# Kernel optimization log

Hardware: AMD Instinct MI355X
Metric: run time of the kernel (lower is better)

The kernel has to match this reference:

```python
import jax, jax.numpy as jnp
import numpy as np

# Geometry constants fixed by the source's index arithmetic
GRID_P, GRID_Q, NUM_ANCH = 60, 40, 9   # p = (i//9)%60, q = i//(60*9), sr = i%9
N = GRID_P * GRID_Q * NUM_ANCH          # 21600 anchors per image
K = 1000                                # top-K candidates kept before NMS
MAX_BOXES = 18                          # fixed output boxes per image
THRESH = 0.5                            # NMS overlap threshold
BATCH = 64


def setup_inputs() -> dict:
    key = jax.random.key(0)
    k1, k2 = jax.random.split(key)
    x = jax.random.normal(k1, (BATCH, N, 6), dtype=jnp.float32)
    # anchor boxes (x, y, w, h); keep w,h strictly positive and away from 0
    anchor_boxes = jax.random.uniform(k2, (GRID_P, GRID_Q, NUM_ANCH, 4),
                                      dtype=jnp.float32, minval=0.05, maxval=1.0)
    return {"x": x, "anchor_boxes": anchor_boxes}


def _per_sample(ypred, anchors):
    scores, order = jax.lax.top_k(ypred[:, 0], K)          # descending, matches tf.argsort DESC [:1000]
    p = (order // NUM_ANCH) % GRID_P
    q = order // (GRID_P * NUM_ANCH)
    sr = order % NUM_ANCH
    a = anchors[p, q, sr]                                   # [K, 4] (xa, ya, wa, ha)
    regr = ypred[order, 2:6]                                # [K, 4] (dx, dy, dw, dh)
    xc = regr[:, 0] * a[:, 2] + a[:, 0]
    yc = regr[:, 1] * a[:, 3] + a[:, 1]
    w = a[:, 2] * jnp.exp(regr[:, 2])
    h = a[:, 3] * jnp.exp(regr[:, 3])
    cand = jnp.stack([xc, yc, w, h, scores], axis=-1)       # [K, 5] xywh+score

    # xywh -> xyxy for overlap computation (as in non_max_suppression_fast)
    x1 = xc - 0.5 * w; x2 = xc + 0.5 * w
    y1 = yc - 0.5 * h; y2 = yc + 0.5 * h
    area = (x2 - x1) * (y2 - y1)                            # [K]

    # pairwise intersection; overlap[i, j] = inter(i, j) / area(j)  (source divides by
    # the area of the lower-scored candidate, NOT the union -- kept faithfully)
    xx1 = jnp.maximum(x1[:, None], x1[None, :])
    yy1 = jnp.maximum(y1[:, None], y1[None, :])
    xx2 = jnp.minimum(x2[:, None], x2[None, :])
    yy2 = jnp.minimum(y2[:, None], y2[None, :])
    iw = jnp.maximum(0.0, xx2 - xx1)
    ih = jnp.maximum(0.0, yy2 - yy1)
    sup = (iw * ih / area[None, :]) > THRESH                # [K, K] bool

    # greedy NMS over candidates in descending-score order
    jrange = jnp.arange(K)
    def body(i, keep):
        return keep & ~(keep[i] & sup[i] & (jrange > i))
    keep = jax.lax.fori_loop(0, K, body, jnp.ones((K,), dtype=bool))

    # pack first MAX_BOXES kept boxes into fixed-shape output
    ranks = jnp.cumsum(keep) - 1                            # position among kept
    valid = keep & (ranks < MAX_BOXES)
    picked = jnp.zeros((MAX_BOXES, 5), cand.dtype).at[
        jnp.where(valid, ranks, MAX_BOXES)
    ].set(jnp.where(valid[:, None], cand, 0.0), mode='drop')

    # pad with top-scored decoded boxes if fewer than MAX_BOXES survive NMS
    n = jnp.minimum(jnp.sum(keep), MAX_BOXES)
    j = jnp.arange(MAX_BOXES)
    pad = cand[jnp.clip(j - n, 0, K - 1)]
    return jnp.where((j < n)[:, None], picked, pad)         # [MAX_BOXES, 5]


def reference(x, anchor_boxes):
    return jax.vmap(lambda y: _per_sample(y, anchor_boxes))(x)  # [B, 18, 5]
```

## Files before the change

### kernel.cpp

```cpp
#include <hip/hip_runtime.h>

#define NELEM 21600
#define KSEL 1000
#define MAXB 18
#define NT 1024
#define CAP 2048
#define NBIN 6144
#define BSHIFT 12
#define NCHUNK 4
#define QC 8100
#define QK 5400
#define NFULL 21
#define NTAIL (NELEM - NFULL * NT)

typedef unsigned long long ull;

__device__ __forceinline__ unsigned fkey(float f) {
  unsigned u = __float_as_uint(f);
  return (u & 0x80000000u) ? ~u : (u | 0x80000000u);
}
__device__ __forceinline__ float unfkey(unsigned k) {
  unsigned u = (k & 0x80000000u) ? (k ^ 0x80000000u) : ~k;
  return __uint_as_float(u);
}

__global__ __launch_bounds__(NT) void k1_scan(
    const float* __restrict__ x, unsigned* __restrict__ gkeys,
    unsigned* __restrict__ ghist, unsigned* __restrict__ gcnt,
    unsigned* __restrict__ gflag) {
  const int blk = blockIdx.x;
  const int s = blk >> 2, c = blk & 3;
  const int t = threadIdx.x;
  const float4* xq = (const float4*)(x + (size_t)s * NELEM * 6);
  unsigned* gk = gkeys + (size_t)s * NELEM;

  __shared__ unsigned h[2048];
  h[2 * t] = 0u; h[2 * t + 1] = 0u;
  if (c == 0 && t == 0) { gcnt[s] = 0u; gflag[s] = 0u; }
  __syncthreads();

  const int base = c * QC;
  #pragma unroll
  for (int k = 0; k < 8; ++k) {
    int off = t + (k << 10);
    if (k < 7 || off < QC) {
      int g = base + off;
      float4 v = xq[g];
      int r = g % 3;
      if (r == 0) {
        unsigned key = fkey(v.x);
        gk[2 * (g / 3)] = key;
        atomicAdd(&h[key >> 21], 1u);
      } else if (r == 1) {
        unsigned key = fkey(v.z);
        gk[2 * (g / 3) + 1] = key;
        atomicAdd(&h[key >> 21], 1u);
      }
    }
  }
  __syncthreads();
  unsigned* gh = ghist + (size_t)blk * 2048;
  gh[2 * t] = h[2 * t];
  gh[2 * t + 1] = h[2 * t + 1];
}

__device__ void select_bucket(const unsigned* hist, unsigned target,
                              volatile unsigned* chunkSuf,
                              unsigned* outB, unsigned* outCnt, unsigned* outAbove) {
  const int tid = threadIdx.x;
  const int w = tid >> 6, l = tid & 63;
  unsigned h1 = hist[w * 128 + 2 * l + 1];
  unsigned s = hist[w * 128 + 2 * l] + h1;
  #pragma unroll
  for (int d = 1; d < 64; d <<= 1) {
    unsigned t = __shfl_down(s, d);
    if (l + d < 64) s += t;
  }
  if (l == 0) chunkSuf[w] = s;
  __syncthreads();
  if (w == 0) {
    unsigned ct = (l < 16) ? chunkSuf[l] : 0u;
    unsigned cs = ct;
    #pragma unroll
    for (int d = 1; d < 16; d <<= 1) {
      unsigned t = __shfl_down(cs, d);
      if (l + d < 16) cs += t;
    }
    if (l < 16) chunkSuf[l] = cs - ct;
  }
  __syncthreads();
  unsigned base = chunkSuf[w];
  unsigned sufE = s + base;
  unsigned sN = __shfl_down(s, 1);
  unsigned sufN = ((l < 63) ? sN : 0u) + base;
  unsigned geOdd = sufN + h1;
  if (sufE >= target && geOdd < target) { *outB = w * 128u + 2u * l;     *outCnt = sufE;  *outAbove = geOdd; }
  if (geOdd >= target && sufN < target) { *outB = w * 128u + 2u * l + 1; *outCnt = geOdd; *outAbove = sufN;  }
  __syncthreads();
}

__global__ __launch_bounds__(NT) void k2_compact(
    const unsigned* __restrict__ gkeys, const unsigned* __restrict__ ghist,
    ull* __restrict__ gselPk, unsigned* __restrict__ gcnt,
    unsigned* __restrict__ gflag, unsigned* __restrict__ gtb) {
  const int blk = blockIdx.x;
  const int s = blk >> 2, q = blk & 3;
  const int tid = threadIdx.x;

  __shared__ unsigned hist[2048];
  __shared__ unsigned chunkSuf[16];
  __shared__ ull lbuf[CAP];
  __shared__ unsigned lcnt, gbase;
  __shared__ unsigned sB, sCnt, sAbove;

  {
    unsigned h0 = 0, h1 = 0;
    #pragma unroll
    for (int c = 0; c < NCHUNK; ++c) {
      const unsigned* gh = ghist + (size_t)(s * NCHUNK + c) * 2048;
      h0 += gh[2 * tid];
      h1 += gh[2 * tid + 1];
    }
    hist[2 * tid] = h0; hist[2 * tid + 1] = h1;
  }
  if (tid == 0) lcnt = 0u;
  __syncthreads();
  select_bucket(hist, KSEL, chunkSuf, &sB, &sCnt, &sAbove);

  if (sCnt > (unsigned)CAP) {
    if (tid == 0 && q == 0) gflag[s] = 1u;
    return;
  }
  const unsigned TB = sB << 21;
  if (tid == 0 && q == 0) gtb[s] = TB;
  const unsigned* ks = gkeys + (size_t)s * NELEM + q * QK;
  const int lw = tid & 63;
  #pragma unroll
  for (int it = 0; it < 6; ++it) {
    int i = tid + (it << 10);
    bool pred = false;
    unsigned k = 0u;
    if (i < QK) { k = ks[i]; pred = (k >= TB); }
    ull mask = __ballot(pred);
    if (mask) {
      int leader = __builtin_ctzll(mask);
      unsigned tot = (unsigned)__popcll(mask);
      unsigned bp = 0;
      if (lw == leader) bp = atomicAdd(&lcnt, tot);
      bp = __shfl(bp, leader);
      if (pred) {
        unsigned p = bp + (unsigned)__popcll(mask & ((1ull << lw) - 1ull));
        unsigned idx = (unsigned)(q * QK + i);
        lbuf[p] = ((ull)k << 32) | (unsigned)(~idx);
      }
    }
  }
  __syncthreads();
  if (tid == 0) gbase = atomicAdd(&gcnt[s], lcnt);
  __syncthreads();
  ull* gs = gselPk + (size_t)s * CAP;
  const unsigned n = lcnt, b0 = gbase;
  for (unsigned i = tid; i < n; i += NT) gs[b0 + i] = lbuf[i];
}

__global__ __launch_bounds__(NT) void k3_final(
    const float* __restrict__ x, const float* __restrict__ anch,
    const unsigned* __restrict__ gkeys, const unsigned* __restrict__ ghist,
    const ull* __restrict__ gselPk, const unsigned* __restrict__ gcnt,
    const unsigned* __restrict__ gflag, const unsigned* __restrict__ gtb,
    float* __restrict__ out) {
  const int s = blockIdx.x;
  const int tid = threadIdx.x;
  const float* xb = x + (size_t)s * NELEM * 6;

  __shared__ ull pkraw[CAP];
  __shared__ ull sorted[CAP];
  __shared__ unsigned hist[NBIN + 2];
  __shared__ unsigned short orig16[NBIN + 2];
  __shared__ float px1[1088], py1[1088], px2[1088], py2[1088];
  __shared__ unsigned chunkSuf[16];
  __shared__ unsigned sB, sCnt, sAbove;
  __shared__ unsigned cntsh;
  __shared__ int keptRank[MAXB];
  __shared__ int numKept;

  unsigned n, TB;
  if (gflag[s] == 0u) {
    n = gcnt[s]; if (n > CAP) n = CAP;
    TB = gtb[s];
    const ull* gs = gselPk + (size_t)s * CAP;
    for (unsigned i = tid; i < n; i += NT) pkraw[i] = gs[i];
  } else {
    const unsigned* ks = gkeys + (size_t)s * NELEM;
    unsigned kv[NFULL];
    #pragma unroll
    for (int u = 0; u < NFULL; ++u) kv[u] = ks[tid + (u << 10)];
    unsigned ktail = 0u;
    const bool hastail = tid < NTAIL;
    if (hastail) ktail = ks[tid + NFULL * NT];
    {
      unsigned h0 = 0, h1 = 0;
      #pragma unroll
      for (int c = 0; c < NCHUNK; ++c) {
        const unsigned* gh = ghist + (size_t)(s * NCHUNK + c) * 2048;
        h0 += gh[2 * tid];
        h1 += gh[2 * tid + 1];
      }
      hist[2 * tid] = h0; hist[2 * tid + 1] = h1;
    }
    __syncthreads();
    select_bucket(hist, KSEL, chunkSuf, &sB, &sCnt, &sAbove);
    const unsigned b1 = sB, above1 = sAbove;
    hist[2 * tid] = 0u; hist[2 * tid + 1] = 0u;
    __syncthreads();
    #pragma unroll
    for (int u = 0; u < NFULL; ++u)
      if ((kv[u] >> 21) == b1) atomicAdd(&hist[(kv[u] >> 10) & 0x7FFu], 1u);
    if (hastail && (ktail >> 21) == b1) atomicAdd(&hist[(ktail >> 10) & 0x7FFu], 1u);
    __syncthreads();
    select_bucket(hist, KSEL - above1, chunkSuf, &sB, &sCnt, &sAbove);
    TB = (b1 << 21) | (sB << 10);
    if (tid == 0) cntsh = 0u;
    __syncthreads();
    const int lw = tid & 63;
    #pragma unroll
    for (int u = 0; u < NFULL; ++u) {
      bool pred = kv[u] >= TB;
      ull mask = __ballot(pred);
      if (mask) {
        int leader = __builtin_ctzll(mask);
        unsigned total = (unsigned)__popcll(mask);
        unsigned basep = 0;
        if (lw == leader) basep = atomicAdd(&cntsh, total);
        basep = __shfl(basep, leader);
        if (pred) {
          unsigned p = basep + (unsigned)__popcll(mask & ((1ull << lw) - 1ull));
          unsigned i = (unsigned)(tid + (u << 10));
          if (p < CAP) pkraw[p] = ((ull)kv[u] << 32) | (unsigned)(~i);
        }
      }
    }
    if (hastail && ktail >= TB) {
      unsigned p = atomicAdd(&cntsh, 1u);
      unsigned i = (unsigned)(tid + NFULL * NT);
      if (p < CAP) pkraw[p] = ((ull)ktail << 32) | (unsigned)(~i);
    }
    __syncthreads();
    n = (cntsh < CAP) ? cntsh : CAP;
  }

  {
    #pragma unroll
    for (int j = 0; j < 6; ++j) hist[tid * 6 + j] = 0u;
    if (tid == 0) { hist[NBIN] = 0u; hist[NBIN + 1] = 0u; }
    __syncthreads();
    #pragma unroll
    for (int e0 = 0; e0 < 2; ++e0) {
      unsigned e = tid + (e0 << 10);
      if (e < n) {
        unsigned key = (unsigned)(pkraw[e] >> 32);
        unsigned bin = (key - TB) >> BSHIFT;
        if (bin > (NBIN - 1)) bin = NBIN - 1;
        atomicAdd(&hist[bin], 1u);
      }
    }
    __syncthreads();
    unsigned c6[6];
    #pragma unroll
    for (int j = 0; j < 6; ++j) c6[j] = hist[tid * 6 + j];
    unsigned part = 0;
    #pragma unroll
    for (int j = 0; j < 6; ++j) part += c6[j];
    const int w = tid >> 6, l = tid & 63;
    unsigned ssum = part;
    #pragma unroll
    for (int d = 1; d < 64; d <<= 1) {
      unsigned t2 = __shfl_down(ssum, d);
      if (l + d < 64) ssum += t2;
    }
    if (l == 0) chunkSuf[w] = ssum;
    __syncthreads();
    if (w == 0) {
      unsigned ct = (l < 16) ? chunkSuf[l] : 0u;
      unsigned cs = ct;
      #pragma unroll
      for (int d = 1; d < 16; d <<= 1) {
        unsigned t2 = __shfl_down(cs, d);
        if (l + d < 16) cs += t2;
      }
      if (l < 16) chunkSuf[l] = cs - ct;
    }
    __syncthreads();
    unsigned after = chunkSuf[w] + (ssum - part);
    unsigned run = after;
    unsigned suf6[6];
    #pragma unroll
    for (int j = 5; j >= 0; --j) { run += c6[j]; suf6[j] = run; }
    __syncthreads();
    #pragma unroll
    for (int j = 0; j < 6; ++j) {
      hist[tid * 6 + j] = suf6[j];
      orig16[tid * 6 + j] = (unsigned short)suf6[j];
    }
    if (tid == 0) { hist[NBIN] = 0u; orig16[NBIN] = 0; }
    __syncthreads();
    #pragma unroll
    for (int e0 = 0; e0 < 2; ++e0) {
      unsigned e = tid + (e0 << 10);
      if (e < n) {
        ull pk = pkraw[e];
        unsigned key = (unsigned)(pk >> 32);
        unsigned bin = (key - TB) >> BSHIFT;
        if (bin > (NBIN - 1)) bin = NBIN - 1;
        unsigned pos = atomicAdd(&hist[bin + 1], 1u);
        sorted[pos] = pk;
      }
    }
    __syncthreads();
    #pragma unroll
    for (int b0 = 0; b0 < 6; ++b0) {
      int b = tid + (b0 << 10);
      if (b < NBIN) {
        int st = orig16[b + 1];
        int en = orig16[b];
        for (int i = st + 1; i < en; ++i) {
          ull v = sorted[i];
          int j = i - 1;
          while (j >= st && sorted[j] < v) { sorted[j + 1] = sorted[j]; --j; }
          sorted[j + 1] = v;
        }
      }
    }
    __syncthreads();
  }

  if (tid < KSEL) {
    unsigned idx = ~(unsigned)sorted[tid];
    const float2* e2 = (const float2*)(xb + (size_t)idx * 6 + 2);
    float2 ra = e2[0], rb = e2[1];
    unsigned pp = (idx / 9u) % 60u;
    unsigned qq = idx / 540u;
    unsigned sr = idx % 9u;
    const float* ap = anch + (((pp * 40u + qq) * 9u + sr) * 4u);
    float ax = ap[0], ay = ap[1], aw = ap[2], ah = ap[3];
    float xc = ra.x * aw + ax;
    float yc = ra.y * ah + ay;
    float w = aw * expf(rb.x);
    float h = ah * expf(rb.y);
    int a = (tid >> 4) * 17 + (tid & 15);
    px1[a] = xc - 0.5f * w; px2[a] = xc + 0.5f * w;
    py1[a] = yc - 0.5f * h; py2[a] = yc + 0.5f * h;
  }
  __syncthreads();

  if (tid < 64) {
    const int lane = tid;
    unsigned alive = 0u;
    #pragma unroll
    for (int ss = 0; ss < 16; ++ss) {
      int r = lane * 16 + ss;
      alive |= (r < KSEL ? 1u : 0u) << ss;
    }
    int nk = 0;
    while (nk < MAXB) {
      ull bal = __ballot(alive != 0u);
      if (!bal) break;
      int F = __builtin_ctzll(bal);
      int myss = (int)__builtin_ctz(alive | 0x10000u);
      int ssw = __shfl(myss, F);
      int m = F * 16 + ssw;
      if (lane == 0) keptRank[nk] = m;
      int am = (m >> 4) * 17 + (m & 15);
      float wx1 = px1[am], wy1 = py1[am], wx2 = px2[am], wy2 = py2[am];
      ++nk;
      if (nk >= MAXB) break;
      #pragma unroll
      for (int ss = 0; ss < 16; ++ss) {
        if (alive & (1u << ss)) {
          int a = lane * 17 + ss;
          float x1 = px1[a], y1 = py1[a], x2 = px2[a], y2 = py2[a];
          float iw = fmaxf(fminf(x2, wx2) - fmaxf(x1, wx1), 0.f);
          float ih = fmaxf(fminf(y2, wy2) - fmaxf(y1, wy1), 0.f);
          float ar = (x2 - x1) * (y2 - y1);
          if (iw * ih / ar > 0.5f) alive &= ~(1u << ss);
        }
      }
    }
    if (lane == 0) numKept = nk;
  }
  __syncthreads();

  const int nK = numKept;
  if (tid < MAXB) {
    int j = tid;
    int r = (j < nK) ? keptRank[j] : (j - nK);
    ull pk = sorted[r];
    unsigned idx = ~(unsigned)pk;
    float sc = unfkey((unsigned)(pk >> 32));
    const float2* e2 = (const float2*)(xb + (size_t)idx * 6 + 2);
    float2 ra = e2[0], rb = e2[1];
    unsigned pp = (idx / 9u) % 60u;
    unsigned qq = idx / 540u;
    unsigned sr = idx % 9u;
    const float* ap = anch + (((pp * 40u + qq) * 9u + sr) * 4u);
    float ax = ap[0], ay = ap[1], aw = ap[2], ah = ap[3];
    float xc = ra.x * aw + ax;
    float yc = ra.y * ah + ay;
    float w = aw * expf(rb.x);
    float h = ah * expf(rb.y);
    float* o = out + s * (MAXB * 5) + j * 5;
    o[0] = xc; o[1] = yc; o[2] = w; o[3] = h; o[4] = sc;
  }
}

extern "C" void kernel_launch(void* const* d_in, const int* in_sizes, int n_in,
                              void* d_out, int out_size, void* d_ws, size_t ws_size,
                              hipStream_t stream) {
  const float* x = (const float*)d_in[0];
  const float* anch = (const float*)d_in[1];
  float* out = (float*)d_out;
  const int B = in_sizes[0] / (NELEM * 6);
  ull* gselPk = (ull*)d_ws;
  unsigned* ghist = (unsigned*)(gselPk + (size_t)B * CAP);
  unsigned* gkeys = ghist + (size_t)B * NCHUNK * 2048;
  unsigned* gcnt = gkeys + (size_t)B * NELEM;
  unsigned* gflag = gcnt + B;
  unsigned* gtb = gflag + B;
  k1_scan<<<dim3(B * NCHUNK), dim3(NT), 0, stream>>>(x, gkeys, ghist, gcnt, gflag);
  k2_compact<<<dim3(B * NCHUNK), dim3(NT), 0, stream>>>(gkeys, ghist, gselPk, gcnt, gflag, gtb);
  k3_final<<<dim3(B), dim3(NT), 0, stream>>>(x, anch, gkeys, ghist, gselPk, gcnt, gflag, gtb, out);
}
```

Baseline: 62.28 us.

## Decode candidate boxes in compaction kernel and carry them through the sort

Candidate boxes are now decoded (gather from x and anchors, plus exp) inside k2_compact, which runs with 4x more blocks, and written to a new workspace array. k3_final loads the predecoded boxes into shared memory and tracks a slot permutation through the bucket/insertion sort, so the NMS setup and output stages no longer perform dependent global gathers. In exchange it decodes every candidate (up to 2048) rather than only the top 1000, adds global traffic for the box array, and raises k3's shared-memory footprint by about 36 KB, which could reduce occupancy.

```diff
diff --git a/kernel.cpp b/kernel.cpp
--- a/kernel.cpp
+++ b/kernel.cpp
@@ -22,6 +22,23 @@
 __device__ __forceinline__ float unfkey(unsigned k) {
   unsigned u = (k & 0x80000000u) ? (k ^ 0x80000000u) : ~k;
   return __uint_as_float(u);
+}
+
+__device__ __forceinline__ float4 decode_box(const float* xb, const float* anch,
+                                             unsigned idx) {
+  const float2* e2 = (const float2*)(xb + (size_t)idx * 6 + 2);
+  float2 ra = e2[0], rb = e2[1];
+  unsigned pp = (idx / 9u) % 60u;
+  unsigned qq = idx / 540u;
+  unsigned sr = idx % 9u;
+  const float* ap = anch + (((pp * 40u + qq) * 9u + sr) * 4u);
+  float ax = ap[0], ay = ap[1], aw = ap[2], ah = ap[3];
+  float4 r;
+  r.x = ra.x * aw + ax;
+  r.y = ra.y * ah + ay;
+  r.z = aw * expf(rb.x);
+  r.w = ah * expf(rb.y);
+  return r;
 }
 
 __global__ __launch_bounds__(NT) void k1_scan(
@@ -100,12 +117,15 @@
 }
 
 __global__ __launch_bounds__(NT) void k2_compact(
+    const float* __restrict__ x, const float* __restrict__ anch,
     const unsigned* __restrict__ gkeys, const unsigned* __restrict__ ghist,
-    ull* __restrict__ gselPk, unsigned* __restrict__ gcnt,
-    unsigned* __restrict__ gflag, unsigned* __restrict__ gtb) {
+    ull* __restrict__ gselPk, float4* __restrict__ gbox,
+    unsigned* __restrict__ gcnt, unsigned* __restrict__ gflag,
+    unsigned* __restrict__ gtb) {
   const int blk = blockIdx.x;
   const int s = blk >> 2, q = blk & 3;
   const int tid = threadIdx.x;
+  const float* xb = x + (size_t)s * NELEM * 6;
 
   __shared__ unsigned hist[2048];
   __shared__ unsigned chunkSuf[16];
@@ -159,22 +179,29 @@
   if (tid == 0) gbase = atomicAdd(&gcnt[s], lcnt);
   __syncthreads();
   ull* gs = gselPk + (size_t)s * CAP;
+  float4* gb = gbox + (size_t)s * CAP;
   const unsigned n = lcnt, b0 = gbase;
-  for (unsigned i = tid; i < n; i += NT) gs[b0 + i] = lbuf[i];
+  for (unsigned i = tid; i < n; i += NT) {
+    ull pk = lbuf[i];
+    gs[b0 + i] = pk;
+    gb[b0 + i] = decode_box(xb, anch, ~(unsigned)pk);
+  }
 }
 
 __global__ __launch_bounds__(NT) void k3_final(
     const float* __restrict__ x, const float* __restrict__ anch,
     const unsigned* __restrict__ gkeys, const unsigned* __restrict__ ghist,
-    const ull* __restrict__ gselPk, const unsigned* __restrict__ gcnt,
-    const unsigned* __restrict__ gflag, const unsigned* __restrict__ gtb,
-    float* __restrict__ out) {
+    const ull* __restrict__ gselPk, const float4* __restrict__ gbox,
+    const unsigned* __restrict__ gcnt, const unsigned* __restrict__ gflag,
+    const unsigned* __restrict__ gtb, float* __restrict__ out) {
   const int s = blockIdx.x;
   const int tid = threadIdx.x;
   const float* xb = x + (size_t)s * NELEM * 6;
 
   __shared__ ull pkraw[CAP];
   __shared__ ull sorted[CAP];
+  __shared__ unsigned short slot16[CAP];
+  __shared__ float4 boxL[CAP];
   __shared__ unsigned hist[NBIN + 2];
   __shared__ unsigned short orig16[NBIN + 2];
   __shared__ float px1[1088], py1[1088], px2[1088], py2[1088];
@@ -189,7 +216,11 @@
     n = gcnt[s]; if (n > CAP) n = CAP;
     TB = gtb[s];
     const ull* gs = gselPk + (size_t)s * CAP;
-    for (unsigned i = tid; i < n; i += NT) pkraw[i] = gs[i];
+    const float4* gb = gbox + (size_t)s * CAP;
+    for (unsigned i = tid; i < n; i += NT) {
+      pkraw[i] = gs[i];
+      boxL[i] = gb[i];
+    }
   } else {
     const unsigned* ks = gkeys + (size_t)s * NELEM;
     unsigned kv[NFULL];
@@ -247,6 +278,8 @@
     }
     __syncthreads();
     n = (cntsh < CAP) ? cntsh : CAP;
+    for (unsigned i = tid; i < n; i += NT)
+      boxL[i] = decode_box(xb, anch, ~(unsigned)pkraw[i]);
   }
 
   {
@@ -314,6 +347,7 @@
         if (bin > (NBIN - 1)) bin = NBIN - 1;
         unsigned pos = atomicAdd(&hist[bin + 1], 1u);
         sorted[pos] = pk;
+        slot16[pos] = (unsigned short)e;
       }
     }
     __syncthreads();
@@ -325,9 +359,15 @@
         int en = orig16[b];
         for (int i = st + 1; i < en; ++i) {
           ull v = sorted[i];
+          unsigned short sv = slot16[i];
           int j = i - 1;
-          while (j >= st && sorted[j] < v) { sorted[j + 1] = sorted[j]; --j; }
+          while (j >= st && sorted[j] < v) {
+            sorted[j + 1] = sorted[j];
+            slot16[j + 1] = slot16[j];
+            --j;
+          }
           sorted[j + 1] = v;
+          slot16[j + 1] = sv;
         }
       }
     }
@@ -335,21 +375,10 @@
   }
 
   if (tid < KSEL) {
-    unsigned idx = ~(unsigned)sorted[tid];
-    const float2* e2 = (const float2*)(xb + (size_t)idx * 6 + 2);
-    float2 ra = e2[0], rb = e2[1];
-    unsigned pp = (idx / 9u) % 60u;
-    unsigned qq = idx / 540u;
-    unsigned sr = idx % 9u;
-    const float* ap = anch + (((pp * 40u + qq) * 9u + sr) * 4u);
-    float ax = ap[0], ay = ap[1], aw = ap[2], ah = ap[3];
-    float xc = ra.x * aw + ax;
-    float yc = ra.y * ah + ay;
-    float w = aw * expf(rb.x);
-    float h = ah * expf(rb.y);
+    float4 b = boxL[slot16[tid]];
     int a = (tid >> 4) * 17 + (tid & 15);
-    px1[a] = xc - 0.5f * w; px2[a] = xc + 0.5f * w;
-    py1[a] = yc - 0.5f * h; py2[a] = yc + 0.5f * h;
+    px1[a] = b.x - 0.5f * b.z; px2[a] = b.x + 0.5f * b.z;
+    py1[a] = b.y - 0.5f * b.w; py2[a] = b.y + 0.5f * b.w;
   }
   __syncthreads();
 
@@ -395,21 +424,10 @@
     int j = tid;
     int r = (j < nK) ? keptRank[j] : (j - nK);
     ull pk = sorted[r];
-    unsigned idx = ~(unsigned)pk;
+    float4 b = boxL[slot16[r]];
     float sc = unfkey((unsigned)(pk >> 32));
-    const float2* e2 = (const float2*)(xb + (size_t)idx * 6 + 2);
-    float2 ra = e2[0], rb = e2[1];
-    unsigned pp = (idx / 9u) % 60u;
-    unsigned qq = idx / 540u;
-    unsigned sr = idx % 9u;
-    const float* ap = anch + (((pp * 40u + qq) * 9u + sr) * 4u);
-    float ax = ap[0], ay = ap[1], aw = ap[2], ah = ap[3];
-    float xc = ra.x * aw + ax;
-    float yc = ra.y * ah + ay;
-    float w = aw * expf(rb.x);
-    float h = ah * expf(rb.y);
     float* o = out + s * (MAXB * 5) + j * 5;
-    o[0] = xc; o[1] = yc; o[2] = w; o[3] = h; o[4] = sc;
+    o[0] = b.x; o[1] = b.y; o[2] = b.z; o[3] = b.w; o[4] = sc;
   }
 }
 
@@ -421,12 +439,13 @@
   float* out = (float*)d_out;
   const int B = in_sizes[0] / (NELEM * 6);
   ull* gselPk = (ull*)d_ws;
-  unsigned* ghist = (unsigned*)(gselPk + (size_t)B * CAP);
+  float4* gbox = (float4*)(gselPk + (size_t)B * CAP);
+  unsigned* ghist = (unsigned*)(gbox + (size_t)B * CAP);
   unsigned* gkeys = ghist + (size_t)B * NCHUNK * 2048;
   unsigned* gcnt = gkeys + (size_t)B * NELEM;
   unsigned* gflag = gcnt + B;
   unsigned* gtb = gflag + B;
   k1_scan<<<dim3(B * NCHUNK), dim3(NT), 0, stream>>>(x, gkeys, ghist, gcnt, gflag);
-  k2_compact<<<dim3(B * NCHUNK), dim3(NT), 0, stream>>>(gkeys, ghist, gselPk, gcnt, gflag, gtb);
-  k3_final<<<dim3(B), dim3(NT), 0, stream>>>(x, anch, gkeys, ghist, gselPk, gcnt, gflag, gtb, out);
-}
+  k2_compact<<<dim3(B * NCHUNK), dim3(NT), 0, stream>>>(x, anch, gkeys, ghist, gselPk, gbox, gcnt, gflag, gtb);
+  k3_final<<<dim3(B), dim3(NT), 0, stream>>>(x, anch, gkeys, ghist, gselPk, gbox, gcnt, gflag, gtb, out);
+}
```

Result: faster. 60.72 us (-2.5%).
